# Performance work log

Measured on AMD Instinct MI355X. Metric: run time of the kernel, lower is better.

## Reference

```python
import jax, jax.numpy as jnp
import numpy as np


def _seg_softmax(e, seg, n):
    m = jax.ops.segment_max(e, seg, num_segments=n)
    ex = jnp.exp(e - m[seg])
    s = jax.ops.segment_sum(ex, seg, num_segments=n)
    return ex / (s[seg] + 1e-16)


def _gat_conv(x, src, dst, ea, W, a_s, a_d, We, a_e, b, heads, C, concat, N):
    # PyG GATConv math (eval mode, no dropout)
    h = (x @ W).reshape(N, heads, C)                    # [N,H,C]
    he = (ea @ We).reshape(-1, heads, C)                # [Ef,H,C]
    al = jnp.sum(h * a_s, -1)[src] + jnp.sum(h * a_d, -1)[dst] + jnp.sum(he * a_e, -1)
    al = jax.nn.leaky_relu(al, 0.2)                     # [Ef,H]
    alpha = _seg_softmax(al, dst, N)
    out = jax.ops.segment_sum(alpha[:, :, None] * h[src], dst, num_segments=N)
    out = out.reshape(N, heads * C) if concat else out.mean(1)
    return out + b


def _ln(x, g, b):
    mu = x.mean(-1, keepdims=True)
    v = x.var(-1, keepdims=True)
    return (x - mu) / jnp.sqrt(v + 1e-5) * g + b


def setup_inputs() -> dict:
    key = jax.random.key(0)
    ks = jax.random.split(key, 20)
    B, L, E_PER = 512, 64, 4
    N = B * L
    E = N * E_PER
    x = jax.random.normal(ks[0], (N, 55), jnp.float32)
    # within-graph random edges (each graph is a contiguous block of L nodes)
    off = (jnp.arange(E) // (L * E_PER)) * L
    src = off + jax.random.randint(ks[1], (E,), 0, L)
    dst = off + jax.random.randint(ks[2], (E,), 0, L)
    edge_index = jnp.stack([src, dst])
    edge_attr = jax.random.uniform(ks[3], (E, 6), dtype=jnp.float32)
    node_gid = jnp.arange(N) // L
    food_ids = jax.random.randint(ks[4], (B,), 0, 29)
    p = lambda i, shape: jax.random.normal(ks[i], shape, jnp.float32) * 0.05
    return dict(
        x=x, edge_attr=edge_attr, edge_index=edge_index, node_gid=node_gid, food_ids=food_ids,
        W1=p(5, (55, 1024)), as1=p(6, (4, 256)), ad1=p(7, (4, 256)),
        We1=p(8, (6, 1024)), ae1=p(9, (4, 256)), b1=jnp.zeros((1024,), jnp.float32),
        g1=jnp.ones((1024,), jnp.float32), be1=jnp.zeros((1024,), jnp.float32),
        W2=p(10, (1024, 256)), as2=p(11, (1, 256)), ad2=p(12, (1, 256)),
        We2=p(13, (6, 256)), ae2=p(14, (1, 256)), b2=jnp.zeros((256,), jnp.float32),
        g2=jnp.ones((256,), jnp.float32), be2=jnp.zeros((256,), jnp.float32),
        Wa=p(15, (256, 256)), va=p(16, (256,)), emb=p(17, (29, 256)))


def reference(x, edge_attr, edge_index, node_gid, food_ids,
              W1, as1, ad1, We1, ae1, b1, g1, be1,
              W2, as2, ad2, We2, ae2, b2, g2, be2,
              Wa, va, emb):
    N = x.shape[0]
    B = food_ids.shape[0]
    src, dst = edge_index[0], edge_index[1]
    # add self loops; self-loop edge_attr = mean of incoming edge attrs (PyG fill_value='mean')
    ones = jnp.ones((src.shape[0],), x.dtype)
    deg = jax.ops.segment_sum(ones, dst, num_segments=N)
    mean_ea = jax.ops.segment_sum(edge_attr, dst, num_segments=N) / jnp.maximum(deg, 1.0)[:, None]
    loop = jnp.arange(N)
    src_f = jnp.concatenate([src, loop])
    dst_f = jnp.concatenate([dst, loop])
    ea_f = jnp.concatenate([edge_attr, mean_ea], 0)
    # GATEncoder
    h = _gat_conv(x, src_f, dst_f, ea_f, W1, as1, ad1, We1, ae1, b1, 4, 256, True, N)
    h = jax.nn.relu(_ln(h, g1, be1))
    h = _gat_conv(h, src_f, dst_f, ea_f, W2, as2, ad2, We2, ae2, b2, 1, 256, False, N)
    h = _ln(h, g2, be2)                                  # [N,256]
    # per-graph attention over nodes, then attention-weighted max-pool
    scores = jnp.tanh(h @ Wa) @ va                       # [N]
    attn = _seg_softmax(scores, node_gid, B)             # [N]
    hw = h * attn[:, None]
    drug_fea = jax.ops.segment_max(hw, node_gid, num_segments=B)[:, None, :]  # [B,1,256]
    food_fea = emb[food_ids][:, None, :]                 # [B,1,256]
    return drug_fea, food_fea, attn
```

## Files before the change

### kernel.cpp

```cpp
#include <hip/hip_runtime.h>
#include <cstdint>
#include <cstddef>


#define LEAKY_SLOPE 0.2f

typedef __attribute__((ext_vector_type(8))) _Float16 half8;
typedef __attribute__((ext_vector_type(4))) float facc4;

__global__ void k_prep_w(const float* __restrict__ W1, const float* __restrict__ W2,
                         const float* __restrict__ Wa,
                         const float* __restrict__ We1, const float* __restrict__ ae1,
                         const float* __restrict__ We2, const float* __restrict__ ae2,
                         const float* __restrict__ as1, const float* __restrict__ ad1,
                         _Float16* __restrict__ w1t, _Float16* __restrict__ w2t,
                         _Float16* __restrict__ wat, float* __restrict__ fold) {
    int idx = blockIdx.x * blockDim.x + threadIdx.x;
    if (idx < 1024 * 64) {
        int c = idx >> 6, k = idx & 63;
        w1t[idx] = (k < 55) ? (_Float16)W1[(size_t)k * 1024 + c] : (_Float16)0.f;
        return;
    }
    idx -= 1024 * 64;
    if (idx < 256 * 1024) {
        int c = idx >> 10, k = idx & 1023;
        w2t[idx] = (_Float16)W2[(size_t)k * 256 + c];
        return;
    }
    idx -= 256 * 1024;
    if (idx < 256 * 256) {
        int c = idx >> 8, k = idx & 255;
        int dst = ((c >> 4) * 8 + (k >> 5)) * 512 + ((c & 15) + 16 * ((k >> 3) & 3)) * 8 + (k & 7);
        wat[dst] = (_Float16)Wa[(size_t)k * 256 + c];
        return;
    }
    int t = idx - 256 * 256;
    if (t < 24) {
        int k = t >> 2, h = t & 3;
        float s = 0.f;
        for (int c = 0; c < 256; ++c) s += We1[k * 1024 + h * 256 + c] * ae1[h * 256 + c];
        fold[t] = s;
    } else if (t < 30) {
        int k = t - 24;
        float s = 0.f;
        for (int c = 0; c < 256; ++c) s += We2[k * 256 + c] * ae2[c];
        fold[32 + k] = s;
    } else if (t >= 64 && t < 284) {
        int i = t - 64, k = i >> 2, h = i & 3;
        float s = 0.f;
        for (int c = 0; c < 256; ++c) s += W1[k * 1024 + h * 256 + c] * as1[h * 256 + c];
        fold[64 + i] = s;
    } else if (t >= 320 && t < 540) {
        int i = t - 320, k = i >> 2, h = i & 3;
        float s = 0.f;
        for (int c = 0; c < 256; ++c) s += W1[k * 1024 + h * 256 + c] * ad1[h * 256 + c];
        fold[320 + i] = s;
    }
}

__global__ void k_prep_x(const float* __restrict__ x, const float* __restrict__ wa1,
                         const float* __restrict__ wd1, _Float16* __restrict__ xbf,
                         float* __restrict__ ss1, float* __restrict__ sd1, int N) {
    int idx = blockIdx.x * blockDim.x + threadIdx.x;
    if (idx < N * 64) {
        int n = idx >> 6, k = idx & 63;
        _Float16 v = (k < 55) ? (_Float16)x[(size_t)n * 55 + k] : (_Float16)0.f;
        int g = n >> 6, nl = n & 63;
        size_t dst = (size_t)g * 4096 +
                     (((k >> 4) * 2 + (nl >> 5)) * 512 +
                      ((k & 15) + 16 * ((nl >> 3) & 3)) * 8 + (nl & 7));
        xbf[dst] = v;
        return;
    }
    int n = idx - N * 64;
    if (n >= N) return;
    float a0 = 0, a1 = 0, a2 = 0, a3 = 0, d0 = 0, d1 = 0, d2 = 0, d3 = 0;
    for (int k = 0; k < 55; ++k) {
        float xv = x[(size_t)n * 55 + k];
        float4 wa = *reinterpret_cast<const float4*>(&wa1[k * 4]);
        float4 wd = *reinterpret_cast<const float4*>(&wd1[k * 4]);
        a0 += xv * wa.x; a1 += xv * wa.y; a2 += xv * wa.z; a3 += xv * wa.w;
        d0 += xv * wd.x; d1 += xv * wd.y; d2 += xv * wd.z; d3 += xv * wd.w;
    }
    *reinterpret_cast<float4*>(&ss1[n * 4]) = make_float4(a0, a1, a2, a3);
    *reinterpret_cast<float4*>(&sd1[n * 4]) = make_float4(d0, d1, d2, d3);
}

__global__ __launch_bounds__(256) void k_graph_csr(
    const int* __restrict__ ei, const float* __restrict__ ea,
    const float* __restrict__ we1, const float* __restrict__ we2,
    int* __restrict__ coff, int* __restrict__ eid,
    float* __restrict__ ead1, float* __restrict__ ead2, int E, int B) {
    __shared__ int degL[64];
    __shared__ float meaL[64][6];
    __shared__ int cs[65];
    __shared__ int fillL[64];
    int g = blockIdx.x;
    int ng = g * 64;
    int e0 = g * 256;
    int tid = threadIdx.x;
    if (tid < 64) {
        degL[tid] = 0; fillL[tid] = 0;
#pragma unroll
        for (int k = 0; k < 6; ++k) meaL[tid][k] = 0.f;
    }
    __syncthreads();
    int eg = e0 + tid;
    int dst = ei[E + eg];
    int dl = dst - ng;
    atomicAdd(&degL[dl], 1);
#pragma unroll
    for (int k = 0; k < 6; ++k) atomicAdd(&meaL[dl][k], ea[(size_t)eg * 6 + k]);
    __syncthreads();
    if (tid < 64) {
        int v = degL[tid] + 1;
        int incl = v;
#pragma unroll
        for (int o = 1; o < 64; o <<= 1) {
            int up = __shfl_up(incl, o);
            if (tid >= o) incl += up;
        }
        cs[tid + 1] = incl;
        if (tid == 0) cs[0] = 0;
        coff[ng + tid] = g * 320 + (incl - v);
        if (g == B - 1 && tid == 63) coff[ng + 64] = (g + 1) * 320;
    }
    __syncthreads();
    {
        float v[4] = {};
        float v2 = 0.f;
        const float* eap = ea + (size_t)eg * 6;
#pragma unroll
        for (int k = 0; k < 6; ++k) {
            float a = eap[k];
#pragma unroll
            for (int h = 0; h < 4; ++h) v[h] += a * we1[k * 4 + h];
            v2 += a * we2[k];
        }
#pragma unroll
        for (int h = 0; h < 4; ++h) ead1[(size_t)eg * 4 + h] = v[h];
        ead2[eg] = v2;
        int pos = cs[dl] + atomicAdd(&fillL[dl], 1);
        eid[g * 320 + pos] = eg;
    }
    if (tid < 64) {
        float inv = 1.f / fmaxf((float)degL[tid], 1.f);
        float v[4] = {};
        float v2 = 0.f;
#pragma unroll
        for (int k = 0; k < 6; ++k) {
            float a = meaL[tid][k] * inv;
#pragma unroll
            for (int h = 0; h < 4; ++h) v[h] += a * we1[k * 4 + h];
            v2 += a * we2[k];
        }
        int se = E + ng + tid;
#pragma unroll
        for (int h = 0; h < 4; ++h) ead1[(size_t)se * 4 + h] = v[h];
        ead2[se] = v2;
        int pos = cs[tid] + atomicAdd(&fillL[tid], 1);
        eid[g * 320 + pos] = se;
    }
}

__global__ __launch_bounds__(512) void k_pbuild1(
    const _Float16* __restrict__ xbf,
    const int* __restrict__ coff, const int* __restrict__ eid, const int* __restrict__ ei,
    const float* __restrict__ ead1, const float* __restrict__ ss1,
    const float* __restrict__ sd1,
    _Float16* __restrict__ XA, int ldxa, int E, int g0) {
    __shared__ _Float16 Pm[4][64 * 64];
    __shared__ float llds[384][4];
    __shared__ int slds[384];
    int g = blockIdx.x;
    int ng = (g0 + g) * 64;
    int lr0 = g * 64;
    int tid = threadIdx.x;
    int lane = tid & 63, wid = tid >> 6;
    int l15 = lane & 15, l4 = lane >> 4;
    for (int i = tid; i < 4 * 64 * 64 / 8; i += 512)
        *reinterpret_cast<int4*>(&Pm[0][0] + i * 8) = int4{0, 0, 0, 0};
    int pbase = coff[ng];
    int pcnt = coff[ng + 64] - pbase;
    if (pcnt > 384) pcnt = 384;
    for (int p = tid; p < pcnt; p += 512) {
        int e = eid[pbase + p];
        int s, d;
        if (e < E) { s = ei[e]; d = ei[E + e]; } else { s = e - E; d = s; }
        slds[p] = s - ng;
        float4 sv = *reinterpret_cast<const float4*>(&ss1[s * 4]);
        float4 dv = *reinterpret_cast<const float4*>(&sd1[d * 4]);
        float4 ev = *reinterpret_cast<const float4*>(&ead1[(size_t)e * 4]);
        float v0 = sv.x + dv.x + ev.x, v1 = sv.y + dv.y + ev.y;
        float v2 = sv.z + dv.z + ev.z, v3 = sv.w + dv.w + ev.w;
        llds[p][0] = (v0 > 0.f) ? v0 : LEAKY_SLOPE * v0;
        llds[p][1] = (v1 > 0.f) ? v1 : LEAKY_SLOPE * v1;
        llds[p][2] = (v2 > 0.f) ? v2 : LEAKY_SLOPE * v2;
        llds[p][3] = (v3 > 0.f) ? v3 : LEAKY_SLOPE * v3;
    }
    __syncthreads();
    if (tid < 256) {
        int dst = tid >> 2, h = tid & 3;
        int p0 = coff[ng + dst] - pbase, p1 = coff[ng + dst + 1] - pbase;
        float m = -1e30f;
        for (int p = p0; p < p1; ++p) m = fmaxf(m, llds[p][h]);
        float sm = 0.f;
        for (int p = p0; p < p1; ++p) sm += expf(llds[p][h] - m);
        float iv = 1.f / (sm + 1e-16f);
        for (int p = p0; p < p1; ++p) {
            int src = slds[p];
            int pos = dst * 64 + (((src >> 3) ^ (dst & 7)) << 3) + (src & 7);
            Pm[h][pos] = (_Float16)((float)Pm[h][pos] + expf(llds[p][h] - m) * iv);
        }
    }
    __syncthreads();
    int head = wid >> 1, fjh = wid & 1;
    const _Float16* xg = xbf + (size_t)(g0 + g) * 4096;
    facc4 acc[4][2] = {};
#pragma unroll
    for (int kk = 0; kk < 2; ++kk) {
        half8 af[4], bf[2];
#pragma unroll
        for (int f = 0; f < 4; ++f) {
            int arow = f * 16 + l15;
            af[f] = *reinterpret_cast<const half8*>(
                &Pm[head][arow * 64 + (((kk * 4 + l4) ^ (arow & 7)) << 3)]);
        }
#pragma unroll
        for (int f = 0; f < 2; ++f)
            bf[f] = *reinterpret_cast<const half8*>(
                xg + (((fjh * 2 + f) * 2 + kk) * 512 + lane * 8));
#pragma unroll
        for (int fi = 0; fi < 4; ++fi)
#pragma unroll
            for (int fj = 0; fj < 2; ++fj)
                acc[fi][fj] = __builtin_amdgcn_mfma_f32_16x16x32_f16(
                    af[fi], bf[fj], acc[fi][fj], 0, 0, 0);
    }
#pragma unroll
    for (int fi = 0; fi < 4; ++fi)
#pragma unroll
        for (int fj = 0; fj < 2; ++fj)
#pragma unroll
            for (int i = 0; i < 4; ++i) {
                int r = fi * 16 + l4 * 4 + i;
                int k2 = fjh * 32 + fj * 16 + l15;
                XA[((size_t)head * ldxa + lr0 + r) * 64 + k2] = (_Float16)acc[fi][fj][i];
            }
}

__global__ __launch_bounds__(256) void k_gemm_heads(
    const _Float16* __restrict__ XA, int ldxa, const _Float16* __restrict__ w1t,
    _Float16* __restrict__ hpre) {
    int h = blockIdx.z;
    const _Float16* A = XA + (size_t)h * ldxa * 64;
    const _Float16* BT = w1t + (size_t)h * 256 * 64;
    __shared__ _Float16 As[128 * 64];
    __shared__ _Float16 Bs[128 * 64];
    int tid = threadIdx.x;
    int lane = tid & 63, wid = tid >> 6;
    int wr = wid >> 1, wc = wid & 1;
    int l15 = lane & 15, l4 = lane >> 4;
    int r0 = blockIdx.y * 128, c0 = blockIdx.x * 128;
    facc4 acc[4][4] = {};
#pragma unroll
    for (int i = 0; i < 4; ++i) {
        int ch = tid + 256 * i;
        int row = ch >> 3, col16 = ch & 7;
        int sw = col16 ^ (row & 7);
        *reinterpret_cast<int4*>(&As[row * 64 + sw * 8]) =
            *reinterpret_cast<const int4*>(A + (size_t)(r0 + row) * 64 + col16 * 8);
        *reinterpret_cast<int4*>(&Bs[row * 64 + sw * 8]) =
            *reinterpret_cast<const int4*>(BT + (size_t)(c0 + row) * 64 + col16 * 8);
    }
    __syncthreads();
#pragma unroll
    for (int kk = 0; kk < 2; ++kk) {
        half8 af[4], bf[4];
#pragma unroll
        for (int f = 0; f < 4; ++f) {
            int arow = wr * 64 + f * 16 + l15;
            int ac = (kk * 4 + l4) ^ (arow & 7);
            af[f] = *reinterpret_cast<const half8*>(&As[arow * 64 + ac * 8]);
            int brow = wc * 64 + f * 16 + l15;
            int bc = (kk * 4 + l4) ^ (brow & 7);
            bf[f] = *reinterpret_cast<const half8*>(&Bs[brow * 64 + bc * 8]);
        }
#pragma unroll
        for (int fi = 0; fi < 4; ++fi)
#pragma unroll
            for (int fj = 0; fj < 4; ++fj)
                acc[fi][fj] = __builtin_amdgcn_mfma_f32_16x16x32_f16(
                    af[fi], bf[fj], acc[fi][fj], 0, 0, 0);
    }
#pragma unroll
    for (int fi = 0; fi < 4; ++fi)
#pragma unroll
        for (int fj = 0; fj < 4; ++fj)
#pragma unroll
            for (int i = 0; i < 4; ++i) {
                int r = r0 + wr * 64 + fi * 16 + l4 * 4 + i;
                int cc = h * 256 + c0 + wc * 64 + fj * 16 + l15;
                hpre[(size_t)r * 1024 + cc] = (_Float16)acc[fi][fj][i];
            }
}

__global__ __launch_bounds__(256) void k_ln1(
    const _Float16* __restrict__ hpre, const float* __restrict__ b1,
    const float* __restrict__ g1, const float* __restrict__ be1,
    _Float16* __restrict__ hln) {
    int row = blockIdx.x * 4 + (threadIdx.x >> 6);
    int lane = threadIdx.x & 63;
    const _Float16* src = hpre + (size_t)row * 1024;
    float v[16];
    half8 h0 = *reinterpret_cast<const half8*>(src + lane * 8);
    half8 h1 = *reinterpret_cast<const half8*>(src + 512 + lane * 8);
    float lsum = 0.f, lsq = 0.f;
#pragma unroll
    for (int j = 0; j < 8; ++j) {
        v[j] = (float)h0[j] + b1[lane * 8 + j];
        v[8 + j] = (float)h1[j] + b1[512 + lane * 8 + j];
    }
#pragma unroll
    for (int j = 0; j < 16; ++j) { lsum += v[j]; lsq += v[j] * v[j]; }
    for (int o = 32; o; o >>= 1) { lsum += __shfl_xor(lsum, o); lsq += __shfl_xor(lsq, o); }
    float mu = lsum * (1.f / 1024.f);
    float var = lsq * (1.f / 1024.f) - mu * mu;
    float rstd = rsqrtf(var + 1e-5f);
    half8 o0, o1;
#pragma unroll
    for (int j = 0; j < 8; ++j) {
        int c = lane * 8 + j;
        o0[j] = (_Float16)fmaxf((v[j] - mu) * rstd * g1[c] + be1[c], 0.f);
    }
#pragma unroll
    for (int j = 0; j < 8; ++j) {
        int c = 512 + lane * 8 + j;
        o1[j] = (_Float16)fmaxf((v[8 + j] - mu) * rstd * g1[c] + be1[c], 0.f);
    }
    *reinterpret_cast<half8*>(hln + (size_t)row * 1024 + lane * 8) = o0;
    *reinterpret_cast<half8*>(hln + (size_t)row * 1024 + 512 + lane * 8) = o1;
}

__global__ __launch_bounds__(512) void k_gemm2(
    const _Float16* __restrict__ A, const _Float16* __restrict__ BT,
    const float* __restrict__ as2, const float* __restrict__ ad2,
    _Float16* __restrict__ h2f, float* __restrict__ ss2, float* __restrict__ sd2,
    int n0) {
    __shared__ _Float16 As[128 * 64];
    __shared__ _Float16 Bs[256 * 64];
    __shared__ float s2L[128], d2L[128];
    int tid = threadIdx.x;
    int lane = tid & 63, wid = tid >> 6;
    int wr = wid >> 2, wc = wid & 3;
    int l15 = lane & 15, l4 = lane >> 4;
    int r0 = blockIdx.x * 128;
    if (tid < 128) { s2L[tid] = 0.f; d2L[tid] = 0.f; }
    facc4 acc[4][4] = {};
    for (int kt = 0; kt < 1024; kt += 64) {
#pragma unroll
        for (int i = 0; i < 2; ++i) {
            int ch = tid + 512 * i;
            int row = ch >> 3, col16 = ch & 7;
            int sw = col16 ^ (row & 7);
            *reinterpret_cast<int4*>(&As[row * 64 + sw * 8]) =
                *reinterpret_cast<const int4*>(A + (size_t)(r0 + row) * 1024 + kt + col16 * 8);
        }
#pragma unroll
        for (int i = 0; i < 4; ++i) {
            int ch = tid + 512 * i;
            int row = ch >> 3, col16 = ch & 7;
            int sw = col16 ^ (row & 7);
            *reinterpret_cast<int4*>(&Bs[row * 64 + sw * 8]) =
                *reinterpret_cast<const int4*>(BT + (size_t)row * 1024 + kt + col16 * 8);
        }
        __syncthreads();
#pragma unroll
        for (int kk = 0; kk < 2; ++kk) {
            half8 af[4], bf[4];
#pragma unroll
            for (int f = 0; f < 4; ++f) {
                int arow = wr * 64 + f * 16 + l15;
                int ac = (kk * 4 + l4) ^ (arow & 7);
                af[f] = *reinterpret_cast<const half8*>(&As[arow * 64 + ac * 8]);
                int brow = wc * 64 + f * 16 + l15;
                int bc = (kk * 4 + l4) ^ (brow & 7);
                bf[f] = *reinterpret_cast<const half8*>(&Bs[brow * 64 + bc * 8]);
            }
#pragma unroll
            for (int fi = 0; fi < 4; ++fi)
#pragma unroll
                for (int fj = 0; fj < 4; ++fj)
                    acc[fi][fj] = __builtin_amdgcn_mfma_f32_16x16x32_f16(
                        af[fi], bf[fj], acc[fi][fj], 0, 0, 0);
        }
        __syncthreads();
    }
#pragma unroll
    for (int fi = 0; fi < 4; ++fi)
#pragma unroll
        for (int i = 0; i < 4; ++i) {
            float s2 = 0.f, d2 = 0.f;
#pragma unroll
            for (int fj = 0; fj < 4; ++fj) {
                int r = r0 + wr * 64 + fi * 16 + l4 * 4 + i;
                int cc = wc * 64 + fj * 16 + l15;
                float v = acc[fi][fj][i];
                int g = r >> 6, nl = r & 63;
                size_t dst = (size_t)g * 16384 +
                             (((cc >> 4) * 2 + (nl >> 5)) * 512 +
                              ((cc & 15) + 16 * ((nl >> 3) & 3)) * 8 + (nl & 7));
                h2f[dst] = (_Float16)v;
                s2 += v * as2[cc];
                d2 += v * ad2[cc];
            }
            s2 += __shfl_xor(s2, 1); d2 += __shfl_xor(d2, 1);
            s2 += __shfl_xor(s2, 2); d2 += __shfl_xor(d2, 2);
            s2 += __shfl_xor(s2, 4); d2 += __shfl_xor(d2, 4);
            s2 += __shfl_xor(s2, 8); d2 += __shfl_xor(d2, 8);
            if (l15 == 0) {
                int rl = wr * 64 + fi * 16 + l4 * 4 + i;
                atomicAdd(&s2L[rl], s2);
                atomicAdd(&d2L[rl], d2);
            }
        }
    __syncthreads();
    if (tid < 128) {
        ss2[n0 + r0 + tid] = s2L[tid];
        sd2[n0 + r0 + tid] = d2L[tid];
    }
}

__global__ __launch_bounds__(512) void k_graph2f(
    const _Float16* __restrict__ h2f,
    const int* __restrict__ coff, const int* __restrict__ eid, const int* __restrict__ ei,
    const float* __restrict__ ead2, const float* __restrict__ ss2g,
    const float* __restrict__ sd2g,
    const float* __restrict__ b2, const float* __restrict__ g2,
    const float* __restrict__ be2,
    const _Float16* __restrict__ wat, const float* __restrict__ va,
    const int* __restrict__ food, const float* __restrict__ emb,
    float* __restrict__ out, int E, int B, int g0) {
    __shared__ _Float16 hfL[64 * 256];
    _Float16* Pm = hfL;
    float* Pf = reinterpret_cast<float*>(hfL + 4096);
    float* llds = reinterpret_cast<float*>(hfL + 12288);
    int* slds = reinterpret_cast<int*>(hfL + 12288 + 640);
    int* dlds = reinterpret_cast<int*>(hfL + 12288 + 1280);
    float* mL  = reinterpret_cast<float*>(hfL + 12288 + 1920);
    float* ivL = reinterpret_cast<float*>(hfL + 12288 + 2048);
    __shared__ float rsum[64], rsq[64];
    __shared__ float part[8][64];
    __shared__ float at[64];
    int g = blockIdx.x;
    int b = g0 + g;
    int ng = (g0 + g) * 64;
    int tid = threadIdx.x;
    int lane = tid & 63, wid = tid >> 6;
    int l15 = lane & 15, l4 = lane >> 4;
    int cbase = wid * 32;
    if (tid < 64) { rsum[tid] = 0.f; rsq[tid] = 0.f; }
    for (int i = tid; i < 1024; i += 512)
        reinterpret_cast<int4*>(Pf)[i] = int4{0, 0, 0, 0};
    const _Float16* hg = h2f + (size_t)g * 16384;
    half8 bfr[2][2];
#pragma unroll
    for (int kk = 0; kk < 2; ++kk)
#pragma unroll
        for (int f = 0; f < 2; ++f)
            bfr[kk][f] = *reinterpret_cast<const half8*>(
                hg + ((((cbase + f * 16) >> 4) * 2 + kk) * 512 + lane * 8));
    int pbase = coff[ng];
    int pcnt = coff[ng + 64] - pbase;
    if (pcnt > 384) pcnt = 384;
    for (int p = tid; p < pcnt; p += 512) {
        int e = eid[pbase + p];
        int s, d;
        if (e < E) { s = ei[e]; d = ei[E + e]; } else { s = e - E; d = s; }
        slds[p] = s - ng;
        dlds[p] = d - ng;
        float v = ss2g[s] + sd2g[d] + ead2[e];
        llds[p] = (v > 0.f) ? v : LEAKY_SLOPE * v;
    }
    __syncthreads();
    {
        int dst = tid >> 3, sub = tid & 7;
        int p0 = coff[ng + dst] - pbase, p1 = coff[ng + dst + 1] - pbase;
        float m = -1e30f;
        for (int p = p0 + sub; p < p1; p += 8) m = fmaxf(m, llds[p]);
        m = fmaxf(m, __shfl_xor(m, 1));
        m = fmaxf(m, __shfl_xor(m, 2));
        m = fmaxf(m, __shfl_xor(m, 4));
        float sm = 0.f;
        for (int p = p0 + sub; p < p1; p += 8) sm += expf(llds[p] - m);
        sm += __shfl_xor(sm, 1);
        sm += __shfl_xor(sm, 2);
        sm += __shfl_xor(sm, 4);
        if (sub == 0) { mL[dst] = m; ivL[dst] = 1.f / (sm + 1e-16f); }
    }
    __syncthreads();
    for (int p = tid; p < pcnt; p += 512) {
        int d = dlds[p];
        int src = slds[p];
        float a = expf(llds[p] - mL[d]) * ivL[d];
        atomicAdd(&Pf[d * 64 + (((src >> 3) ^ (d & 7)) << 3) + (src & 7)], a);
    }
    __syncthreads();
    {
        float4 a = reinterpret_cast<const float4*>(Pf)[tid * 2];
        float4 c = reinterpret_cast<const float4*>(Pf)[tid * 2 + 1];
        half8 o;
        o[0] = (_Float16)a.x; o[1] = (_Float16)a.y; o[2] = (_Float16)a.z; o[3] = (_Float16)a.w;
        o[4] = (_Float16)c.x; o[5] = (_Float16)c.y; o[6] = (_Float16)c.z; o[7] = (_Float16)c.w;
        __syncthreads();
        *reinterpret_cast<half8*>(&Pm[tid * 8]) = o;
    }
    __syncthreads();
    facc4 acc[4][2] = {};
#pragma unroll
    for (int kk = 0; kk < 2; ++kk) {
        half8 af[4];
#pragma unroll
        for (int f = 0; f < 4; ++f) {
            int arow = f * 16 + l15;
            af[f] = *reinterpret_cast<const half8*>(
                &Pm[arow * 64 + (((kk * 4 + l4) ^ (arow & 7)) << 3)]);
        }
#pragma unroll
        for (int fi = 0; fi < 4; ++fi)
#pragma unroll
            for (int fj = 0; fj < 2; ++fj)
                acc[fi][fj] = __builtin_amdgcn_mfma_f32_16x16x32_f16(
                    af[fi], bfr[kk][fj], acc[fi][fj], 0, 0, 0);
    }
    float bb[2];
#pragma unroll
    for (int fj = 0; fj < 2; ++fj) bb[fj] = b2[cbase + fj * 16 + l15];
#pragma unroll
    for (int fi = 0; fi < 4; ++fi)
#pragma unroll
        for (int i = 0; i < 4; ++i) {
            float s = 0.f, q = 0.f;
#pragma unroll
            for (int fj = 0; fj < 2; ++fj) {
                float v = acc[fi][fj][i] + bb[fj];
                acc[fi][fj][i] = v;
                s += v; q += v * v;
            }
            s += __shfl_xor(s, 1); q += __shfl_xor(q, 1);
            s += __shfl_xor(s, 2); q += __shfl_xor(q, 2);
            s += __shfl_xor(s, 4); q += __shfl_xor(q, 4);
            s += __shfl_xor(s, 8); q += __shfl_xor(q, 8);
            if (l15 == 0) {
                int r = fi * 16 + l4 * 4 + i;
                atomicAdd(&rsum[r], s);
                atomicAdd(&rsq[r], q);
            }
        }
    __syncthreads();
#pragma unroll
    for (int fi = 0; fi < 4; ++fi)
#pragma unroll
        for (int i = 0; i < 4; ++i) {
            int rl = l4 * 4 + i;
            float mu = rsum[fi * 16 + rl] * (1.f / 256.f);
            float var = rsq[fi * 16 + rl] * (1.f / 256.f) - mu * mu;
            float rstd = rsqrtf(var + 1e-5f);
#pragma unroll
            for (int fj = 0; fj < 2; ++fj) {
                int c = cbase + fj * 16 + l15;
                float v = (acc[fi][fj][i] - mu) * rstd * g2[c] + be2[c];
                acc[fi][fj][i] = v;
                int idx = (fi * 8 + wid) * 512 +
                          ((fj * 2 + (l15 >> 3)) * 16 + rl) * 8 + (l15 & 7);
                hfL[idx] = (_Float16)v;
            }
        }
    __syncthreads();
    facc4 acc2[4][2] = {};
#pragma unroll
    for (int kk = 0; kk < 8; ++kk) {
        half8 af[4], bf[2];
#pragma unroll
        for (int f = 0; f < 4; ++f)
            af[f] = *reinterpret_cast<const half8*>(&hfL[(f * 8 + kk) * 512 + lane * 8]);
#pragma unroll
        for (int f = 0; f < 2; ++f)
            bf[f] = *reinterpret_cast<const half8*>(
                wat + (((wid * 2 + f) * 8 + kk) * 512 + lane * 8));
#pragma unroll
        for (int fi = 0; fi < 4; ++fi)
#pragma unroll
            for (int fj = 0; fj < 2; ++fj)
                acc2[fi][fj] = __builtin_amdgcn_mfma_f32_16x16x32_f16(
                    af[fi], bf[fj], acc2[fi][fj], 0, 0, 0);
    }
    float vac[2];
#pragma unroll
    for (int fj = 0; fj < 2; ++fj) vac[fj] = va[cbase + fj * 16 + l15];
#pragma unroll
    for (int fi = 0; fi < 4; ++fi)
#pragma unroll
        for (int i = 0; i < 4; ++i) {
            float v = tanhf(acc2[fi][0][i]) * vac[0] + tanhf(acc2[fi][1][i]) * vac[1];
            v += __shfl_xor(v, 1); v += __shfl_xor(v, 2);
            v += __shfl_xor(v, 4); v += __shfl_xor(v, 8);
            if (l15 == 0) part[wid][fi * 16 + l4 * 4 + i] = v;
        }
    __syncthreads();
    if (tid < 64) {
        float sc = part[0][tid] + part[1][tid] + part[2][tid] + part[3][tid] +
                   part[4][tid] + part[5][tid] + part[6][tid] + part[7][tid];
        float m = sc;
        for (int o = 32; o; o >>= 1) m = fmaxf(m, __shfl_xor(m, o));
        float ex = expf(sc - m);
        float s = ex;
        for (int o = 32; o; o >>= 1) s += __shfl_xor(s, o);
        float a = ex / (s + 1e-16f);
        at[tid] = a;
        out[(size_t)B * 512 + (size_t)b * 64 + tid] = a;
    }
    __syncthreads();
#pragma unroll
    for (int fj = 0; fj < 2; ++fj) {
        float m = -1e30f;
#pragma unroll
        for (int fi = 0; fi < 4; ++fi)
#pragma unroll
            for (int i = 0; i < 4; ++i) {
                int r = fi * 16 + l4 * 4 + i;
                m = fmaxf(m, acc[fi][fj][i] * at[r]);
            }
        m = fmaxf(m, __shfl_xor(m, 16));
        m = fmaxf(m, __shfl_xor(m, 32));
        if (l4 == 0)
            out[(size_t)b * 256 + cbase + fj * 16 + l15] = m;
    }
    if (tid < 256)
        out[(size_t)B * 256 + (size_t)b * 256 + tid] =
            emb[(size_t)food[b] * 256 + tid];
}

extern "C" void kernel_launch(void* const* d_in, const int* in_sizes, int n_in,
                              void* d_out, int out_size, void* d_ws, size_t ws_size,
                              hipStream_t stream) {
    const float* x   = (const float*)d_in[0];
    const float* ea  = (const float*)d_in[1];
    const int*   ei  = (const int*)d_in[2];
    const int*   food= (const int*)d_in[4];
    const float* W1  = (const float*)d_in[5];
    const float* as1 = (const float*)d_in[6];
    const float* ad1 = (const float*)d_in[7];
    const float* We1 = (const float*)d_in[8];
    const float* ae1 = (const float*)d_in[9];
    const float* b1  = (const float*)d_in[10];
    const float* g1  = (const float*)d_in[11];
    const float* be1 = (const float*)d_in[12];
    const float* W2  = (const float*)d_in[13];
    const float* as2 = (const float*)d_in[14];
    const float* ad2 = (const float*)d_in[15];
    const float* We2 = (const float*)d_in[16];
    const float* ae2 = (const float*)d_in[17];
    const float* b2  = (const float*)d_in[18];
    const float* g2  = (const float*)d_in[19];
    const float* be2 = (const float*)d_in[20];
    const float* Wa  = (const float*)d_in[21];
    const float* va  = (const float*)d_in[22];
    const float* emb = (const float*)d_in[23];
    float* out = (float*)d_out;

    const int N  = in_sizes[0] / 55;
    const int E  = in_sizes[2] / 2;
    const int B  = in_sizes[4];
    const int Ef = E + N;
    const int LPG = N / B;

    char* w = (char*)d_ws;
    size_t off = 0;
    auto take = [&](size_t bytes) -> char* {
        char* p = w + off;
        off = (off + bytes + 255) & ~(size_t)255;
        return p;
    };
    int*      coff = (int*)take((size_t)(N + 1) * 4);
    int*      eid  = (int*)take((size_t)Ef * 4);
    float*    ead1 = (float*)take((size_t)Ef * 4 * 4);
    float*    ead2 = (float*)take((size_t)Ef * 4);
    float*    fold = (float*)take(4096 * 4);
    float*    ss1  = (float*)take((size_t)N * 4 * 4);
    float*    sd1  = (float*)take((size_t)N * 4 * 4);
    float*    ss2  = (float*)take((size_t)N * 4);
    float*    sd2  = (float*)take((size_t)N * 4);
    _Float16* xbf  = (_Float16*)take((size_t)N * 64 * 2);
    _Float16* w1t  = (_Float16*)take((size_t)1024 * 64 * 2);
    _Float16* w2t  = (_Float16*)take((size_t)256 * 1024 * 2);
    _Float16* wat  = (_Float16*)take((size_t)256 * 256 * 2);
    size_t smallEnd = off;

    int G = B;
    while (G > 2 && smallEnd + (size_t)G * 32768 + 2ull * G * 131072 + 768 > ws_size) G >>= 1;
    _Float16* XA   = (_Float16*)take((size_t)G * 32768);
    _Float16* hpre = (_Float16*)take((size_t)G * 131072);
    _Float16* hln  = (_Float16*)take((size_t)G * 131072);
    _Float16* h2f  = (_Float16*)hpre;

    k_prep_w<<<(1024 * 64 + 256 * 1024 + 256 * 256 + 3072 + 255) / 256, 256, 0, stream>>>(
        W1, W2, Wa, We1, ae1, We2, ae2, as1, ad1, w1t, w2t, wat, fold);
    k_prep_x<<<(N * 64 + N + 255) / 256, 256, 0, stream>>>(
        x, fold + 64, fold + 320, xbf, ss1, sd1, N);
    k_graph_csr<<<B, 256, 0, stream>>>(ei, ea, fold, fold + 32, coff, eid,
                                       ead1, ead2, E, B);

    for (int g0 = 0; g0 < B; g0 += G) {
        int Gc = (g0 + G <= B) ? G : (B - g0);
        int n0 = g0 * LPG;
        int NC = Gc * LPG;
        k_pbuild1<<<Gc, 512, 0, stream>>>(xbf, coff, eid, ei, ead1, ss1, sd1,
                                          XA, NC, E, g0);
        k_gemm_heads<<<dim3(2, NC / 128, 4), 256, 0, stream>>>(XA, NC, w1t, hpre);
        k_ln1<<<NC / 4, 256, 0, stream>>>(hpre, b1, g1, be1, hln);
        k_gemm2<<<NC / 128, 512, 0, stream>>>(hln, w2t, as2, ad2, h2f, ss2, sd2, n0);
        k_graph2f<<<Gc, 512, 0, stream>>>(h2f, coff, eid, ei, ead2, ss2, sd2,
                                          b2, g2, be2, wat, va, food, emb,
                                          out, E, B, g0);
    }
}
```

Before: 151.8 us.

## Fuse LayerNorm1 into GEMM epilogue stats and GEMM2 prologue

The standalone LayerNorm kernel is removed. The head GEMM now adds the bias and accumulates per-row sum and sum of squares with shuffles and atomics. GEMM2 normalizes, scales and ReLUs the A tile while loading it into shared memory. This drops one full read and write of the N×1024 fp16 intermediate and one kernel launch. In exchange it adds float atomics, two memsets per chunk, and a workspace allocation layout that now uses a separate h2f buffer; the per-element g1/be1 loads in the GEMM2 inner load loop also add some work.

```diff
diff --git a/kernel.cpp b/kernel.cpp
--- a/kernel.cpp
+++ b/kernel.cpp
@@ -251,7 +251,8 @@
 
 __global__ __launch_bounds__(256) void k_gemm_heads(
     const _Float16* __restrict__ XA, int ldxa, const _Float16* __restrict__ w1t,
-    _Float16* __restrict__ hpre) {
+    const float* __restrict__ b1, _Float16* __restrict__ hpre,
+    float* __restrict__ rsum, float* __restrict__ rsq) {
     int h = blockIdx.z;
     const _Float16* A = XA + (size_t)h * ldxa * 64;
     const _Float16* BT = w1t + (size_t)h * 256 * 64;
@@ -293,69 +294,53 @@
                 acc[fi][fj] = __builtin_amdgcn_mfma_f32_16x16x32_f16(
                     af[fi], bf[fj], acc[fi][fj], 0, 0, 0);
     }
+    float bb[4];
+#pragma unroll
+    for (int fj = 0; fj < 4; ++fj) bb[fj] = b1[h * 256 + c0 + wc * 64 + fj * 16 + l15];
 #pragma unroll
     for (int fi = 0; fi < 4; ++fi)
 #pragma unroll
-        for (int fj = 0; fj < 4; ++fj)
-#pragma unroll
-            for (int i = 0; i < 4; ++i) {
-                int r = r0 + wr * 64 + fi * 16 + l4 * 4 + i;
+        for (int i = 0; i < 4; ++i) {
+            int r = r0 + wr * 64 + fi * 16 + l4 * 4 + i;
+            float s = 0.f, q = 0.f;
+#pragma unroll
+            for (int fj = 0; fj < 4; ++fj) {
                 int cc = h * 256 + c0 + wc * 64 + fj * 16 + l15;
-                hpre[(size_t)r * 1024 + cc] = (_Float16)acc[fi][fj][i];
-            }
+                float v = acc[fi][fj][i] + bb[fj];
+                hpre[(size_t)r * 1024 + cc] = (_Float16)v;
+                s += v; q += v * v;
+            }
+            s += __shfl_xor(s, 1); q += __shfl_xor(q, 1);
+            s += __shfl_xor(s, 2); q += __shfl_xor(q, 2);
+            s += __shfl_xor(s, 4); q += __shfl_xor(q, 4);
+            s += __shfl_xor(s, 8); q += __shfl_xor(q, 8);
+            if (l15 == 0) { atomicAdd(&rsum[r], s); atomicAdd(&rsq[r], q); }
+        }
 }
 
-__global__ __launch_bounds__(256) void k_ln1(
-    const _Float16* __restrict__ hpre, const float* __restrict__ b1,
+__global__ __launch_bounds__(512) void k_gemm2(
+    const _Float16* __restrict__ hpre, const _Float16* __restrict__ BT,
+    const float* __restrict__ rsum, const float* __restrict__ rsq,
     const float* __restrict__ g1, const float* __restrict__ be1,
-    _Float16* __restrict__ hln) {
-    int row = blockIdx.x * 4 + (threadIdx.x >> 6);
-    int lane = threadIdx.x & 63;
-    const _Float16* src = hpre + (size_t)row * 1024;
-    float v[16];
-    half8 h0 = *reinterpret_cast<const half8*>(src + lane * 8);
-    half8 h1 = *reinterpret_cast<const half8*>(src + 512 + lane * 8);
-    float lsum = 0.f, lsq = 0.f;
-#pragma unroll
-    for (int j = 0; j < 8; ++j) {
-        v[j] = (float)h0[j] + b1[lane * 8 + j];
-        v[8 + j] = (float)h1[j] + b1[512 + lane * 8 + j];
-    }
-#pragma unroll
-    for (int j = 0; j < 16; ++j) { lsum += v[j]; lsq += v[j] * v[j]; }
-    for (int o = 32; o; o >>= 1) { lsum += __shfl_xor(lsum, o); lsq += __shfl_xor(lsq, o); }
-    float mu = lsum * (1.f / 1024.f);
-    float var = lsq * (1.f / 1024.f) - mu * mu;
-    float rstd = rsqrtf(var + 1e-5f);
-    half8 o0, o1;
-#pragma unroll
-    for (int j = 0; j < 8; ++j) {
-        int c = lane * 8 + j;
-        o0[j] = (_Float16)fmaxf((v[j] - mu) * rstd * g1[c] + be1[c], 0.f);
-    }
-#pragma unroll
-    for (int j = 0; j < 8; ++j) {
-        int c = 512 + lane * 8 + j;
-        o1[j] = (_Float16)fmaxf((v[8 + j] - mu) * rstd * g1[c] + be1[c], 0.f);
-    }
-    *reinterpret_cast<half8*>(hln + (size_t)row * 1024 + lane * 8) = o0;
-    *reinterpret_cast<half8*>(hln + (size_t)row * 1024 + 512 + lane * 8) = o1;
-}
-
-__global__ __launch_bounds__(512) void k_gemm2(
-    const _Float16* __restrict__ A, const _Float16* __restrict__ BT,
     const float* __restrict__ as2, const float* __restrict__ ad2,
     _Float16* __restrict__ h2f, float* __restrict__ ss2, float* __restrict__ sd2,
     int n0) {
     __shared__ _Float16 As[128 * 64];
     __shared__ _Float16 Bs[256 * 64];
-    __shared__ float s2L[128], d2L[128];
+    __shared__ float mus[128], rstds[128], s2L[128], d2L[128];
     int tid = threadIdx.x;
     int lane = tid & 63, wid = tid >> 6;
     int wr = wid >> 2, wc = wid & 3;
     int l15 = lane & 15, l4 = lane >> 4;
     int r0 = blockIdx.x * 128;
-    if (tid < 128) { s2L[tid] = 0.f; d2L[tid] = 0.f; }
+    if (tid < 128) {
+        float mu = rsum[r0 + tid] * (1.f / 1024.f);
+        float var = rsq[r0 + tid] * (1.f / 1024.f) - mu * mu;
+        mus[tid] = mu;
+        rstds[tid] = rsqrtf(var + 1e-5f);
+        s2L[tid] = 0.f; d2L[tid] = 0.f;
+    }
+    __syncthreads();
     facc4 acc[4][4] = {};
     for (int kt = 0; kt < 1024; kt += 64) {
 #pragma unroll
@@ -363,8 +348,16 @@
             int ch = tid + 512 * i;
             int row = ch >> 3, col16 = ch & 7;
             int sw = col16 ^ (row & 7);
-            *reinterpret_cast<int4*>(&As[row * 64 + sw * 8]) =
-                *reinterpret_cast<const int4*>(A + (size_t)(r0 + row) * 1024 + kt + col16 * 8);
+            half8 hv = *reinterpret_cast<const half8*>(
+                hpre + (size_t)(r0 + row) * 1024 + kt + col16 * 8);
+            float mu = mus[row], rs = rstds[row];
+            half8 ov;
+#pragma unroll
+            for (int j = 0; j < 8; ++j) {
+                int c = kt + col16 * 8 + j;
+                ov[j] = (_Float16)fmaxf(((float)hv[j] - mu) * rs * g1[c] + be1[c], 0.f);
+            }
+            *reinterpret_cast<half8*>(&As[row * 64 + sw * 8]) = ov;
         }
 #pragma unroll
         for (int i = 0; i < 4; ++i) {
@@ -691,6 +684,8 @@
     float*    sd1  = (float*)take((size_t)N * 4 * 4);
     float*    ss2  = (float*)take((size_t)N * 4);
     float*    sd2  = (float*)take((size_t)N * 4);
+    float*    rsum = (float*)take((size_t)N * 4);
+    float*    rsq  = (float*)take((size_t)N * 4);
     _Float16* xbf  = (_Float16*)take((size_t)N * 64 * 2);
     _Float16* w1t  = (_Float16*)take((size_t)1024 * 64 * 2);
     _Float16* w2t  = (_Float16*)take((size_t)256 * 1024 * 2);
@@ -701,8 +696,7 @@
     while (G > 2 && smallEnd + (size_t)G * 32768 + 2ull * G * 131072 + 768 > ws_size) G >>= 1;
     _Float16* XA   = (_Float16*)take((size_t)G * 32768);
     _Float16* hpre = (_Float16*)take((size_t)G * 131072);
-    _Float16* hln  = (_Float16*)take((size_t)G * 131072);
-    _Float16* h2f  = (_Float16*)hpre;
+    _Float16* h2f  = (_Float16*)take((size_t)G * 131072);
 
     k_prep_w<<<(1024 * 64 + 256 * 1024 + 256 * 256 + 3072 + 255) / 256, 256, 0, stream>>>(
         W1, W2, Wa, We1, ae1, We2, ae2, as1, ad1, w1t, w2t, wat, fold);
@@ -715,11 +709,14 @@
         int Gc = (g0 + G <= B) ? G : (B - g0);
         int n0 = g0 * LPG;
         int NC = Gc * LPG;
+        hipMemsetAsync(rsum, 0, (size_t)NC * 4, stream);
+        hipMemsetAsync(rsq, 0, (size_t)NC * 4, stream);
         k_pbuild1<<<Gc, 512, 0, stream>>>(xbf, coff, eid, ei, ead1, ss1, sd1,
                                           XA, NC, E, g0);
-        k_gemm_heads<<<dim3(2, NC / 128, 4), 256, 0, stream>>>(XA, NC, w1t, hpre);
-        k_ln1<<<NC / 4, 256, 0, stream>>>(hpre, b1, g1, be1, hln);
-        k_gemm2<<<NC / 128, 512, 0, stream>>>(hln, w2t, as2, ad2, h2f, ss2, sd2, n0);
+        k_gemm_heads<<<dim3(2, NC / 128, 4), 256, 0, stream>>>(XA, NC, w1t, b1,
+                                                               hpre, rsum, rsq);
+        k_gemm2<<<NC / 128, 512, 0, stream>>>(hpre, w2t, rsum, rsq, g1, be1,
+                                              as2, ad2, h2f, ss2, sd2, n0);
         k_graph2f<<<Gc, 512, 0, stream>>>(h2f, coff, eid, ei, ead2, ss2, sd2,
                                           b2, g2, be2, wat, va, food, emb,
                                           out, E, B, g0);
```

Measured after the change: 154.7 us. About the same (+1.9%).
